# Kernel optimization log

Hardware: AMD Instinct MI355X
Metric: run time of the kernel (lower is better)

Reference implementation:

```python
import jax, jax.numpy as jnp
import numpy as np

B, L, H, NH, HD, DI, NL = 8, 4096, 256, 4, 64, 1024, 6
_SCALE = 1.0 / np.sqrt(HD).astype(np.float32)


def _layernorm(x, g, b, eps=1e-5):
    m = x.mean(-1, keepdims=True)
    v = ((x - m) ** 2).mean(-1, keepdims=True)
    return (x - m) / jnp.sqrt(v + eps) * g + b


def _forward(data, mask, pos_emb, ln_g, ln_b, ff_w1, ff_b1, ff_w2, ff_b2,
             ff_lng, ff_lnb, ring_wq, ring_bq, ring_wk, ring_bk, ring_wv,
             ring_bv, ring_wo, ring_bo, star_wq, star_bq, star_wk, star_bk,
             star_wv, star_bv, star_wo, star_bo):
    pad = ~mask                                         # [B,L] True = padding
    spad = jnp.concatenate([jnp.zeros((B, 1), bool), pad], axis=1)  # [B,L+1]
    x = data + pos_emb[None, :L]                        # [B,L,H] (emb dropout = eval identity)
    nodes = x
    relay = x.mean(axis=1)                              # [B,H]
    for i in range(NL):
        # --- PositionwiseFeedForward (1x1 conv == dense over channels) ---
        h = nodes
        t = jax.nn.relu(h @ ff_w1[i].T + ff_b1[i]) @ ff_w2[i].T + ff_b2[i]
        h = _layernorm(t + h, ff_lng[i], ff_lnb[i])     # [B,L,H]
        # --- ring attention (_MSA1): size-3 sliding window + global relay key ---
        q = (h @ ring_wq[i].T + ring_bq[i]).reshape(B, L, NH, HD)
        k = (h @ ring_wk[i].T + ring_bk[i]).reshape(B, L, NH, HD)
        v = (h @ ring_wv[i].T + ring_bv[i]).reshape(B, L, NH, HD)
        kp = jnp.pad(k, ((0, 0), (1, 1), (0, 0), (0, 0)))  # zero pad, matches F.unfold
        vp = jnp.pad(v, ((0, 0), (1, 1), (0, 0), (0, 0)))
        k_win = jnp.stack([kp[:, 0:L], kp[:, 1:L + 1], kp[:, 2:L + 2]], axis=2)  # [B,L,3,NH,HD]
        v_win = jnp.stack([vp[:, 0:L], vp[:, 1:L + 1], vp[:, 2:L + 2]], axis=2)
        ak = (relay @ ring_wk[i].T + ring_bk[i]).reshape(B, 1, 1, NH, HD)
        av = (relay @ ring_wv[i].T + ring_bv[i]).reshape(B, 1, 1, NH, HD)
        k_all = jnp.concatenate([k_win, jnp.broadcast_to(ak, (B, L, 1, NH, HD))], axis=2)
        v_all = jnp.concatenate([v_win, jnp.broadcast_to(av, (B, L, 1, NH, HD))], axis=2)
        scores = jnp.einsum('blnd,blwnd->blwn', q, k_all) * _SCALE
        alphas = jax.nn.softmax(scores, axis=2)         # softmax over window dim (4)
        att = jnp.einsum('blwn,blwnd->blnd', alphas, v_all).reshape(B, L, NH * HD)
        ring_out = att @ ring_wo[i].T + ring_bo[i]
        nodes = jax.nn.leaky_relu(_layernorm(ring_out, ln_g[i], ln_b[i]))
        # --- star attention (_MSA2): relay attends to [relay; nodes] ---
        y = jnp.concatenate([relay[:, None, :], nodes], axis=1)  # [B,L+1,H]
        sq = (relay @ star_wq[i].T + star_bq[i]).reshape(B, NH, HD)
        sk = (y @ star_wk[i].T + star_bk[i]).reshape(B, L + 1, NH, HD)
        sv = (y @ star_wv[i].T + star_bv[i]).reshape(B, L + 1, NH, HD)
        s = jnp.einsum('bnd,blnd->bnl', sq, sk) * _SCALE
        s = jnp.where(spad[:, None, :], -jnp.inf, s)
        a = jax.nn.softmax(s, axis=-1)
        satt = jnp.einsum('bnl,blnd->bnd', a, sv).reshape(B, NH * HD)
        relay = jax.nn.leaky_relu(satt @ star_wo[i].T + star_bo[i])
        nodes = jnp.where(pad[:, :, None], 0.0, nodes)
    return nodes, relay


def setup_inputs() -> dict:
    key = jax.random.key(0)
    ks = iter(jax.random.split(key, 64))
    p = lambda shape: jax.random.normal(next(ks), shape, jnp.float32) * 0.02
    C = NH * HD
    return dict(
        data=jax.random.normal(next(ks), (B, L, H), jnp.float32),
        mask=jnp.ones((B, L), bool),
        pos_emb=p((L, H)),
        ln_g=jnp.ones((NL, H), jnp.float32), ln_b=jnp.zeros((NL, H), jnp.float32),
        ff_w1=p((NL, DI, H)), ff_b1=jnp.zeros((NL, DI), jnp.float32),
        ff_w2=p((NL, H, DI)), ff_b2=jnp.zeros((NL, H), jnp.float32),
        ff_lng=jnp.ones((NL, H), jnp.float32), ff_lnb=jnp.zeros((NL, H), jnp.float32),
        ring_wq=p((NL, C, H)), ring_bq=jnp.zeros((NL, C), jnp.float32),
        ring_wk=p((NL, C, H)), ring_bk=jnp.zeros((NL, C), jnp.float32),
        ring_wv=p((NL, C, H)), ring_bv=jnp.zeros((NL, C), jnp.float32),
        ring_wo=p((NL, H, C)), ring_bo=jnp.zeros((NL, H), jnp.float32),
        star_wq=p((NL, C, H)), star_bq=jnp.zeros((NL, C), jnp.float32),
        star_wk=p((NL, C, H)), star_bk=jnp.zeros((NL, C), jnp.float32),
        star_wv=p((NL, C, H)), star_bv=jnp.zeros((NL, C), jnp.float32),
        star_wo=p((NL, H, C)), star_bo=jnp.zeros((NL, H), jnp.float32),
    )


def reference(data, mask, pos_emb, ln_g, ln_b, ff_w1, ff_b1, ff_w2, ff_b2,
              ff_lng, ff_lnb, ring_wq, ring_bq, ring_wk, ring_bk, ring_wv,
              ring_bv, ring_wo, ring_bo, star_wq, star_bq, star_wk, star_bk,
              star_wv, star_bv, star_wo, star_bo):
    return _forward(data, mask, pos_emb, ln_g, ln_b, ff_w1, ff_b1, ff_w2,
                    ff_b2, ff_lng, ff_lnb, ring_wq, ring_bq, ring_wk, ring_bk,
                    ring_wv, ring_bv, ring_wo, ring_bo, star_wq, star_bq,
                    star_wk, star_bk, star_wv, star_bv, star_wo, star_bo)
```

## Files before the change

### kernel.cpp

```cpp
#include <hip/hip_runtime.h>
#include <hip/hip_bf16.h>

#define B_ 8
#define L_ 4096
#define H_ 256
#define NH_ 4
#define DI_ 1024
#define NL_ 6
#define TOK_ (B_*L_)

typedef unsigned short u16;
typedef __attribute__((ext_vector_type(8))) short short8;
typedef __attribute__((ext_vector_type(4))) float f32x4;

struct __align__(8) u16x4 { u16 x,y,z,w; };

__device__ __forceinline__ float bf2f(u16 u){
  union { unsigned u; float f; } c; c.u = ((unsigned)u)<<16; return c.f;
}
__device__ __forceinline__ u16 f2bf(float f){
  union { float f; unsigned u; } c; c.f = f;
  unsigned r = c.u + 0x7FFF + ((c.u>>16)&1);
  return (u16)(r>>16);
}
__device__ __forceinline__ void gload_lds16(const short* g, short* l){
  __builtin_amdgcn_global_load_lds(
      (const __attribute__((address_space(1))) void*)g,
      (__attribute__((address_space(3))) void*)l, 16, 0, 0);
}
__device__ __forceinline__ void block_sync(){
  asm volatile("" ::: "memory");
  __builtin_amdgcn_s_barrier();
  __builtin_amdgcn_sched_barrier(0);
}
#define WAIT_VMCNT(N) asm volatile("s_waitcnt vmcnt(" #N ")" ::: "memory")
#define WAIT_LGKM0()  asm volatile("s_waitcnt lgkmcnt(0)" ::: "memory")

template<bool RELU, bool OBF16>
__global__ __launch_bounds__(512, 4) void gemm_bt(
    const u16* __restrict__ A, const u16* __restrict__ W,
    const float* __restrict__ bias, void* __restrict__ out, int N, int K, int nbn)
{
  constexpr int BM=128, BK=64;
  __shared__ __align__(16) short As[2][BM*BK];
  __shared__ __align__(16) short Ws[2][BM*BK];
  const int tid = threadIdx.x, lane = tid&63, wid = tid>>6;
  const int wm = wid>>1, wn = wid&1;
  const int id = blockIdx.x;
  const int xcd = id & 7, j = id >> 3;
  const int bm = xcd*32 + j / nbn;
  const int bn = j % nbn;
  const short* Ag = (const short*)A + (size_t)bm*BM*K;
  const short* Wg = (const short*)W + (size_t)bn*BM*K;
  f32x4 acc[2][4] = {};

  auto STAGE = [&](int k0, int buf){
    #pragma unroll
    for (int jj=0;jj<2;++jj){
      int c = jj*512 + tid;
      int row = c>>3;
      int col = (c&7) ^ (row&7);
      const size_t src = (size_t)row*K + k0 + col*8;
      gload_lds16(Ag + src, &As[buf][(size_t)c*8]);
      gload_lds16(Wg + src, &Ws[buf][(size_t)c*8]);
    }
  };
  auto COMPUTE = [&](int cur){
    #pragma unroll
    for (int kk=0;kk<BK;kk+=32){
      short8 af[2], bfr[4];
      int kc = (kk>>3) + (lane>>4);
      #pragma unroll
      for (int ms=0;ms<2;++ms){
        int r = wm*32 + ms*16 + (lane&15);
        af[ms] = *(const short8*)&As[cur][r*BK + ((kc ^ (r&7))<<3)];
      }
      #pragma unroll
      for (int ns=0;ns<4;++ns){
        int r = wn*64 + ns*16 + (lane&15);
        bfr[ns] = *(const short8*)&Ws[cur][r*BK + ((kc ^ (r&7))<<3)];
      }
      #pragma unroll
      for (int ms=0;ms<2;++ms)
        #pragma unroll
        for (int ns=0;ns<4;++ns)
          acc[ms][ns] = __builtin_amdgcn_mfma_f32_16x16x32_bf16(af[ms], bfr[ns], acc[ms][ns], 0, 0, 0);
    }
  };

  const int NT = K/BK;
  STAGE(0, 0); STAGE(BK, 1);
  WAIT_VMCNT(4);
  block_sync();
  for (int t=0;t<NT;++t){
    const int cur = t&1;
    __builtin_amdgcn_s_setprio(1);
    COMPUTE(cur);
    __builtin_amdgcn_s_setprio(0);
    block_sync();
    if (t+2 < NT) STAGE((t+2)*BK, cur);
    if (t+1 < NT){
      if (t+2 < NT) { WAIT_VMCNT(4); }
      else          { WAIT_VMCNT(0); }
      block_sync();
    }
  }
  if (OBF16){
    constexpr int OP = 136;
    u16* O = (u16*)&As[0][0];
    #pragma unroll
    for (int ns=0;ns<4;++ns){
      int lc = wn*64 + ns*16 + (lane&15);
      float bc = bias[bn*BM + lc];
      #pragma unroll
      for (int ms=0;ms<2;++ms){
        int rbase = wm*32 + ms*16 + ((lane>>4)<<2);
        #pragma unroll
        for (int i=0;i<4;++i){
          float v = acc[ms][ns][i] + bc;
          if (RELU) v = fmaxf(v, 0.f);
          O[(rbase+i)*OP + lc] = f2bf(v);
        }
      }
    }
    block_sync();
    u16* ob = (u16*)out + (size_t)bm*BM*N + bn*BM;
    const int rr = tid>>4;
    const int cc = (tid&15)<<3;
    #pragma unroll
    for (int p=0;p<4;++p){
      int r = p*32 + rr;
      *reinterpret_cast<short8*>(ob + (size_t)r*N + cc) =
          *reinterpret_cast<const short8*>(&O[r*OP + cc]);
    }
  } else {
    const int r0 = bm*BM + wm*32;
    const int c0 = bn*BM + wn*64;
    #pragma unroll
    for (int ns=0;ns<4;++ns){
      int col = c0 + ns*16 + (lane&15);
      float bc = bias[col];
      #pragma unroll
      for (int ms=0;ms<2;++ms){
        int rbase = r0 + ms*16 + ((lane>>4)<<2);
        #pragma unroll
        for (int i=0;i<4;++i){
          float v = acc[ms][ns][i] + bc;
          if (RELU) v = fmaxf(v, 0.f);
          ((float*)out)[(size_t)(rbase+i)*N + col] = v;
        }
      }
    }
  }
}

template<bool ADDRES, bool LEAKY>
__global__ __launch_bounds__(512, 4) void gemm_ln(
    const u16* __restrict__ A, const u16* __restrict__ W,
    const float* __restrict__ bias, const u16* __restrict__ res,
    const float* __restrict__ g, const float* __restrict__ bv,
    u16* __restrict__ outb, float* __restrict__ outf, int K)
{
  constexpr int BM=64, BK=64;
  __shared__ __align__(16) short As[2][BM*BK];
  __shared__ __align__(16) short Ws[2][256*BK];
  float* S1  = (float*)&As[0][0];
  float* S2  = S1 + 64*4;
  float* MU  = S2 + 64*4;
  float* RSD = MU + 64;
  const int tid = threadIdx.x, lane = tid&63, wid = tid>>6;
  const int wm = wid>>2, wn = wid&3;
  const int m0 = blockIdx.x*BM;
  const short* Ag = (const short*)A + (size_t)m0*K;
  const short* Wg = (const short*)W;
  f32x4 acc[2][4] = {};

  auto STAGE = [&](int k0, int buf){
    {
      int c = tid;
      int row = c>>3;
      int col = (c&7) ^ (row&7);
      gload_lds16(Ag + (size_t)row*K + k0 + col*8, &As[buf][(size_t)c*8]);
    }
    #pragma unroll
    for (int jj=0;jj<4;++jj){
      int c = jj*512 + tid;
      int row = c>>3;
      int col = (c&7) ^ (row&7);
      gload_lds16(Wg + (size_t)row*K + k0 + col*8, &Ws[buf][(size_t)c*8]);
    }
  };
  auto COMPUTE = [&](int cur){
    #pragma unroll
    for (int kk=0;kk<BK;kk+=32){
      short8 af[2], bfr[4];
      int kc = (kk>>3) + (lane>>4);
      #pragma unroll
      for (int ms=0;ms<2;++ms){
        int r = wm*32 + ms*16 + (lane&15);
        af[ms] = *(const short8*)&As[cur][r*BK + ((kc ^ (r&7))<<3)];
      }
      #pragma unroll
      for (int ns=0;ns<4;++ns){
        int r = wn*64 + ns*16 + (lane&15);
        bfr[ns] = *(const short8*)&Ws[cur][r*BK + ((kc ^ (r&7))<<3)];
      }
      #pragma unroll
      for (int ms=0;ms<2;++ms)
        #pragma unroll
        for (int ns=0;ns<4;++ns)
          acc[ms][ns] = __builtin_amdgcn_mfma_f32_16x16x32_bf16(af[ms], bfr[ns], acc[ms][ns], 0, 0, 0);
    }
  };

  const int NT = K/BK;
  STAGE(0, 0); STAGE(BK, 1);
  WAIT_VMCNT(5);
  block_sync();
  for (int t=0;t<NT;++t){
    const int cur = t&1;
    __builtin_amdgcn_s_setprio(1);
    COMPUTE(cur);
    __builtin_amdgcn_s_setprio(0);
    block_sync();
    if (t+2 < NT) STAGE((t+2)*BK, cur);
    if (t+1 < NT){
      if (t+2 < NT) { WAIT_VMCNT(5); }
      else          { WAIT_VMCNT(0); }
      block_sync();
    }
  }
  #pragma unroll
  for (int ns=0;ns<4;++ns){
    int col = wn*64 + ns*16 + (lane&15);
    float bc = bias[col];
    #pragma unroll
    for (int ms=0;ms<2;++ms){
      int rl = wm*32 + ms*16 + ((lane>>4)<<2);
      #pragma unroll
      for (int i=0;i<4;++i){
        float v = acc[ms][ns][i] + bc;
        if (ADDRES) v += bf2f(res[(size_t)(m0+rl+i)*256 + col]);
        acc[ms][ns][i] = v;
      }
    }
  }
  #pragma unroll
  for (int ms=0;ms<2;++ms)
    #pragma unroll
    for (int i=0;i<4;++i){
      float p1 = acc[ms][0][i]+acc[ms][1][i]+acc[ms][2][i]+acc[ms][3][i];
      float p2 = acc[ms][0][i]*acc[ms][0][i] + acc[ms][1][i]*acc[ms][1][i]
               + acc[ms][2][i]*acc[ms][2][i] + acc[ms][3][i]*acc[ms][3][i];
      #pragma unroll
      for (int o=1;o<16;o<<=1){ p1 += __shfl_xor(p1,o,64); p2 += __shfl_xor(p2,o,64); }
      if ((lane&15)==0){
        int rl = wm*32 + ms*16 + ((lane>>4)<<2) + i;
        S1[rl*4 + wn] = p1; S2[rl*4 + wn] = p2;
      }
    }
  __syncthreads();
  if (tid < 64){
    float s1 = S1[tid*4+0]+S1[tid*4+1]+S1[tid*4+2]+S1[tid*4+3];
    float s2 = S2[tid*4+0]+S2[tid*4+1]+S2[tid*4+2]+S2[tid*4+3];
    float mean = s1*(1.f/256.f);
    float var = fmaxf(s2*(1.f/256.f) - mean*mean, 0.f);
    MU[tid] = mean; RSD[tid] = 1.f/sqrtf(var + 1e-5f);
  }
  __syncthreads();
  constexpr int OP = 268;
  u16* O = (u16*)&Ws[0][0];
  #pragma unroll
  for (int ns=0;ns<4;++ns){
    int col = wn*64 + ns*16 + (lane&15);
    float gg = g[col], bb = bv[col];
    #pragma unroll
    for (int ms=0;ms<2;++ms){
      int rl = wm*32 + ms*16 + ((lane>>4)<<2);
      #pragma unroll
      for (int i=0;i<4;++i){
        float y = (acc[ms][ns][i] - MU[rl+i])*RSD[rl+i]*gg + bb;
        if (LEAKY) y = y>0.f ? y : 0.01f*y;
        O[(rl+i)*OP + col] = f2bf(y);
        if (outf) outf[(size_t)(m0+rl+i)*256 + col] = y;
      }
    }
  }
  __syncthreads();
  u16* ob = outb + (size_t)m0*256;
  const int rr = tid>>5;
  const int cc = (tid&31)<<3;
  #pragma unroll
  for (int p=0;p<4;++p){
    int r = p*16 + rr;
    *reinterpret_cast<short8*>(ob + ((size_t)r<<8) + cc) =
        *reinterpret_cast<const short8*>(&O[r*OP + cc]);
  }
}

__global__ __launch_bounds__(512, 4) void attn_ln(
    const u16* __restrict__ qkv, const float* __restrict__ akav,
    const u16* __restrict__ W, const float* __restrict__ bo,
    const float* __restrict__ g, const float* __restrict__ bv,
    u16* __restrict__ outb, float* __restrict__ outf)
{
  constexpr int BK=32, NT=256/BK;
  __shared__ __align__(16) char LB[74240];
  short* Afull = (short*)LB;
  short* Ws2   = (short*)(LB + 32768);
  float* S1  = (float*)(LB + 65536);
  float* S2  = S1 + 256;
  float* MU  = S2 + 256;
  float* RSD = MU + 64;
  const int tid = threadIdx.x, lane = tid&63, wid = tid>>6;
  const int wm = wid>>2, wn = wid&3;
  const int m0 = blockIdx.x*64;
  const short* Wg = (const short*)W;

  auto STAGE_W = [&](int k0, int buf){
    #pragma unroll
    for (int jj=0;jj<2;++jj){
      int c = jj*512 + tid;
      int row = c>>2;
      int col = (c&3) ^ (row&3);
      gload_lds16(Wg + (size_t)row*256 + k0 + col*8, &Ws2[(size_t)buf*8192 + (size_t)c*8]);
    }
  };

  STAGE_W(0, 0); STAGE_W(BK, 1);
  __builtin_amdgcn_sched_barrier(0);

  for (int it=0; it<8; ++it){
    const int rl = wid*8 + it;
    const size_t tok = (size_t)(m0 + rl);
    const int l = (int)(tok & (L_-1));
    const int b = (int)(tok >> 12);
    float q[4], kp[4], kc[4], kn[4], ak[4], vp[4], vc[4], vn[4], av[4];
    u16x4 t4 = *(const u16x4*)(qkv + tok*768 + lane*4);
    q[0]=bf2f(t4.x); q[1]=bf2f(t4.y); q[2]=bf2f(t4.z); q[3]=bf2f(t4.w);
    t4 = *(const u16x4*)(qkv + tok*768 + 256 + lane*4);
    kc[0]=bf2f(t4.x); kc[1]=bf2f(t4.y); kc[2]=bf2f(t4.z); kc[3]=bf2f(t4.w);
    t4 = *(const u16x4*)(qkv + tok*768 + 512 + lane*4);
    vc[0]=bf2f(t4.x); vc[1]=bf2f(t4.y); vc[2]=bf2f(t4.z); vc[3]=bf2f(t4.w);
    if (l>0){
      t4 = *(const u16x4*)(qkv + (tok-1)*768 + 256 + lane*4);
      kp[0]=bf2f(t4.x); kp[1]=bf2f(t4.y); kp[2]=bf2f(t4.z); kp[3]=bf2f(t4.w);
      t4 = *(const u16x4*)(qkv + (tok-1)*768 + 512 + lane*4);
      vp[0]=bf2f(t4.x); vp[1]=bf2f(t4.y); vp[2]=bf2f(t4.z); vp[3]=bf2f(t4.w);
    } else { kp[0]=kp[1]=kp[2]=kp[3]=0.f; vp[0]=vp[1]=vp[2]=vp[3]=0.f; }
    if (l<L_-1){
      t4 = *(const u16x4*)(qkv + (tok+1)*768 + 256 + lane*4);
      kn[0]=bf2f(t4.x); kn[1]=bf2f(t4.y); kn[2]=bf2f(t4.z); kn[3]=bf2f(t4.w);
      t4 = *(const u16x4*)(qkv + (tok+1)*768 + 512 + lane*4);
      vn[0]=bf2f(t4.x); vn[1]=bf2f(t4.y); vn[2]=bf2f(t4.z); vn[3]=bf2f(t4.w);
    } else { kn[0]=kn[1]=kn[2]=kn[3]=0.f; vn[0]=vn[1]=vn[2]=vn[3]=0.f; }
    float4 f4 = ((const float4*)(akav + (size_t)b*H_))[lane];
    ak[0]=f4.x; ak[1]=f4.y; ak[2]=f4.z; ak[3]=f4.w;
    f4 = ((const float4*)(akav + 2048 + (size_t)b*H_))[lane];
    av[0]=f4.x; av[1]=f4.y; av[2]=f4.z; av[3]=f4.w;
    float dp=0.f, dc=0.f, dn=0.f, da=0.f;
    #pragma unroll
    for (int jc=0;jc<4;++jc){ dp += q[jc]*kp[jc]; dc += q[jc]*kc[jc]; dn += q[jc]*kn[jc]; da += q[jc]*ak[jc]; }
    #pragma unroll
    for (int o=1;o<16;o<<=1){
      dp += __shfl_xor(dp,o,64); dc += __shfl_xor(dc,o,64);
      dn += __shfl_xor(dn,o,64); da += __shfl_xor(da,o,64);
    }
    dp *= 0.125f; dc *= 0.125f; dn *= 0.125f; da *= 0.125f;
    float m = fmaxf(fmaxf(dp,dc), fmaxf(dn,da));
    float e0 = expf(dp-m), e1 = expf(dc-m), e2 = expf(dn-m), e3 = expf(da-m);
    float rd = 1.f/(e0+e1+e2+e3);
    u16x4 o4;
    o4.x = f2bf((e0*vp[0]+e1*vc[0]+e2*vn[0]+e3*av[0])*rd);
    o4.y = f2bf((e0*vp[1]+e1*vc[1]+e2*vn[1]+e3*av[1])*rd);
    o4.z = f2bf((e0*vp[2]+e1*vc[2]+e2*vn[2]+e3*av[2])*rd);
    o4.w = f2bf((e0*vp[3]+e1*vc[3]+e2*vn[3]+e3*av[3])*rd);
    int gq = lane>>1;
    int s = (gq & ~7) | ((gq&7) ^ (rl&7));
    *(u16x4*)&Afull[rl*256 + s*8 + (lane&1)*4] = o4;
  }
  WAIT_LGKM0();
  WAIT_VMCNT(2);
  block_sync();

  f32x4 acc[2][4] = {};
  for (int t=0;t<NT;++t){
    const int cur = t&1;
    __builtin_amdgcn_s_setprio(1);
    {
      short8 af[2], bfr[4];
      #pragma unroll
      for (int ms=0;ms<2;++ms){
        int r = wm*32 + ms*16 + (lane&15);
        int gk = t*4 + (lane>>4);
        int s = (gk & ~7) | ((gk&7) ^ (r&7));
        af[ms] = *(const short8*)&Afull[r*256 + s*8];
      }
      #pragma unroll
      for (int ns=0;ns<4;++ns){
        int r2 = wn*64 + ns*16 + (lane&15);
        int sl = (lane>>4) ^ (r2&3);
        bfr[ns] = *(const short8*)&Ws2[(size_t)cur*8192 + r2*32 + sl*8];
      }
      #pragma unroll
      for (int ms=0;ms<2;++ms)
        #pragma unroll
        for (int ns=0;ns<4;++ns)
          acc[ms][ns] = __builtin_amdgcn_mfma_f32_16x16x32_bf16(af[ms], bfr[ns], acc[ms][ns], 0, 0, 0);
    }
    __builtin_amdgcn_s_setprio(0);
    block_sync();
    if (t+2 < NT) STAGE_W((t+2)*BK, cur);
    if (t+1 < NT){
      if (t+2 < NT) { WAIT_VMCNT(2); }
      else          { WAIT_VMCNT(0); }
      block_sync();
    }
  }

  #pragma unroll
  for (int ns=0;ns<4;++ns){
    int col = wn*64 + ns*16 + (lane&15);
    float bc = bo[col];
    #pragma unroll
    for (int ms=0;ms<2;++ms)
      #pragma unroll
      for (int i=0;i<4;++i)
        acc[ms][ns][i] += bc;
  }
  #pragma unroll
  for (int ms=0;ms<2;++ms)
    #pragma unroll
    for (int i=0;i<4;++i){
      float p1 = acc[ms][0][i]+acc[ms][1][i]+acc[ms][2][i]+acc[ms][3][i];
      float p2 = acc[ms][0][i]*acc[ms][0][i] + acc[ms][1][i]*acc[ms][1][i]
               + acc[ms][2][i]*acc[ms][2][i] + acc[ms][3][i]*acc[ms][3][i];
      #pragma unroll
      for (int o=1;o<16;o<<=1){ p1 += __shfl_xor(p1,o,64); p2 += __shfl_xor(p2,o,64); }
      if ((lane&15)==0){
        int rl = wm*32 + ms*16 + ((lane>>4)<<2) + i;
        S1[rl*4 + wn] = p1; S2[rl*4 + wn] = p2;
      }
    }
  __syncthreads();
  if (tid < 64){
    float s1 = S1[tid*4+0]+S1[tid*4+1]+S1[tid*4+2]+S1[tid*4+3];
    float s2 = S2[tid*4+0]+S2[tid*4+1]+S2[tid*4+2]+S2[tid*4+3];
    float mean = s1*(1.f/256.f);
    float var = fmaxf(s2*(1.f/256.f) - mean*mean, 0.f);
    MU[tid] = mean; RSD[tid] = 1.f/sqrtf(var + 1e-5f);
  }
  __syncthreads();
  constexpr int OP = 268;
  u16* O = (u16*)LB;
  #pragma unroll
  for (int ns=0;ns<4;++ns){
    int col = wn*64 + ns*16 + (lane&15);
    float gg = g[col], bb = bv[col];
    #pragma unroll
    for (int ms=0;ms<2;++ms){
      int rl = wm*32 + ms*16 + ((lane>>4)<<2);
      #pragma unroll
      for (int i=0;i<4;++i){
        float y = (acc[ms][ns][i] - MU[rl+i])*RSD[rl+i]*gg + bb;
        y = y>0.f ? y : 0.01f*y;
        O[(rl+i)*OP + col] = f2bf(y);
        if (outf) outf[(size_t)(m0+rl+i)*256 + col] = y;
      }
    }
  }
  __syncthreads();
  u16* ob = outb + (size_t)m0*256;
  const int rr = tid>>5, cc = (tid&31)<<3;
  #pragma unroll
  for (int p=0;p<4;++p){
    int r = p*16 + rr;
    *reinterpret_cast<short8*>(ob + ((size_t)r<<8) + cc) =
        *reinterpret_cast<const short8*>(&O[r*OP + cc]);
  }
}

__global__ __launch_bounds__(256) void star_scores(
    const u16* __restrict__ skv, const float* __restrict__ sq,
    const float* __restrict__ sk0, float* __restrict__ s)
{
  const int g = blockIdx.x*4 + (threadIdx.x>>6);
  if (g >= B_*(L_+1)) return;
  const int lane = threadIdx.x & 63;
  const int b = g/(L_+1), j = g%(L_+1);
  float4 qv = ((const float4*)(sq + (size_t)b*H_))[lane];
  float k0,k1,k2,k3;
  if (j==0){
    float4 kv = ((const float4*)(sk0 + (size_t)b*H_))[lane];
    k0=kv.x; k1=kv.y; k2=kv.z; k3=kv.w;
  } else {
    u16x4 t = *(const u16x4*)(skv + ((size_t)b*L_ + (j-1))*512 + lane*4);
    k0=bf2f(t.x); k1=bf2f(t.y); k2=bf2f(t.z); k3=bf2f(t.w);
  }
  float d = qv.x*k0 + qv.y*k1 + qv.z*k2 + qv.w*k3;
  #pragma unroll
  for (int o=1;o<16;o<<=1) d += __shfl_xor(d,o,64);
  if ((lane&15)==0)
    s[(size_t)(b*4 + (lane>>4))*(L_+1) + j] = d*0.125f;
}

__global__ __launch_bounds__(1024) void star_softmax(float* __restrict__ s)
{
  const int bh = blockIdx.x;
  float* row = s + (size_t)bh*(L_+1);
  __shared__ float red[1024];
  const int tid = threadIdx.x;
  float m = -1e30f;
  for (int j=tid; j<L_+1; j+=1024) m = fmaxf(m, row[j]);
  red[tid] = m; __syncthreads();
  for (int st=512; st>0; st>>=1){ if (tid<st) red[tid] = fmaxf(red[tid], red[tid+st]); __syncthreads(); }
  m = red[0]; __syncthreads();
  float sum = 0.f;
  for (int j=tid; j<L_+1; j+=1024){ float e = expf(row[j]-m); row[j] = e; sum += e; }
  red[tid] = sum; __syncthreads();
  for (int st=512; st>0; st>>=1){ if (tid<st) red[tid] += red[tid+st]; __syncthreads(); }
  const float rs = 1.f/red[0];
  for (int j=tid; j<L_+1; j+=1024) row[j] *= rs;
}

__global__ __launch_bounds__(256) void star_satt_part(
    const float* __restrict__ a, const u16* __restrict__ skv, float* __restrict__ part)
{
  const int blk = blockIdx.x;
  const int b = blk >> 6, seg = blk & 63;
  const int tid = threadIdx.x, q4 = tid & 63, sub = tid >> 6;
  const int h = q4 >> 4;
  const float* arow = a + (size_t)(b*4 + h)*(L_+1) + 1;
  float a0=0.f,a1=0.f,a2=0.f,a3=0.f;
  const int j0 = seg*64 + sub*16;
  #pragma unroll 4
  for (int jj=j0; jj<j0+16; ++jj){
    u16x4 v = *(const u16x4*)(skv + ((size_t)b*L_ + jj)*512 + 256 + q4*4);
    float al = arow[jj];
    a0 += al*bf2f(v.x); a1 += al*bf2f(v.y); a2 += al*bf2f(v.z); a3 += al*bf2f(v.w);
  }
  __shared__ float red[4][256];
  red[sub][q4*4+0]=a0; red[sub][q4*4+1]=a1; red[sub][q4*4+2]=a2; red[sub][q4*4+3]=a3;
  __syncthreads();
  if (sub==0){
    #pragma unroll
    for (int c=0;c<4;++c){
      int ch = q4*4+c;
      part[(size_t)blk*256 + ch] = red[0][ch]+red[1][ch]+red[2][ch]+red[3][ch];
    }
  }
}

__global__ __launch_bounds__(256) void pack_wT(
    const float* __restrict__ w0, const float* __restrict__ w1,
    const float* __restrict__ w2, const float* __restrict__ w3,
    const float* __restrict__ w4, const float* __restrict__ w5,
    float* __restrict__ T)
{
  __shared__ float tile[32][33];
  const int blk = blockIdx.x;
  const int t = blk & 63, m = blk >> 6;
  const int l = m / 6, w = m % 6;
  const float* srcs[6] = {w0, w1, w2, w3, w4, w5};
  const float* src = srcs[w] + (size_t)l*65536;
  const int r0 = (t>>3)*32, c0 = (t&7)*32;
  const int rr = threadIdx.x >> 5, cc = threadIdx.x & 31;
  #pragma unroll
  for (int p=0;p<4;++p)
    tile[rr + p*8][cc] = src[(size_t)(r0 + rr + p*8)*256 + c0 + cc];
  __syncthreads();
  float* dst = T + (size_t)m*65536;
  #pragma unroll
  for (int p=0;p<4;++p)
    dst[(size_t)(c0 + rr + p*8)*256 + r0 + cc] = tile[cc][rr + p*8];
}

struct TPB { const float* b; float* out; };
struct TPB5 { TPB p[5]; };
__global__ __launch_bounds__(256) void relay_projs(
    const float* __restrict__ relay, const float* __restrict__ TW, TPB5 tp)
{
  const int b = blockIdx.x, w = blockIdx.y, n = threadIdx.x;
  __shared__ float rs[H_];
  rs[n] = relay[b*H_ + n];
  __syncthreads();
  const float* wt = TW + (size_t)w*65536;
  float s = tp.p[w].b[n];
  #pragma unroll 8
  for (int c=0;c<H_;++c) s += rs[c]*wt[(size_t)c*256 + n];
  tp.p[w].out[b*H_+n] = s;
}

__global__ __launch_bounds__(256) void relay_tail_k(
    const float* __restrict__ part, const float* __restrict__ a,
    const float* __restrict__ sv0, const float* __restrict__ TW,
    const float* __restrict__ bo, float* __restrict__ relay, float* __restrict__ outr)
{
  const int b = blockIdx.x, n = threadIdx.x;
  __shared__ float rs[H_];
  const int h = n >> 6;
  float s = a[(size_t)(b*4+h)*(L_+1)] * sv0[b*H_ + n];
  #pragma unroll 8
  for (int g2=0; g2<64; ++g2) s += part[((size_t)b*64+g2)*256 + n];
  rs[n] = s;
  __syncthreads();
  const float* wt = TW + (size_t)5*65536;
  float v = bo[n];
  #pragma unroll 8
  for (int c=0;c<H_;++c) v += rs[c]*wt[(size_t)c*256 + n];
  v = v>0.f ? v : 0.01f*v;
  relay[b*H_+n] = v;
  if (outr) outr[b*H_+n] = v;
}

__global__ void f32_to_bf16_k(const float* __restrict__ s, u16* __restrict__ d, int n){
  for (int i = blockIdx.x*blockDim.x + threadIdx.x; i < n; i += gridDim.x*blockDim.x)
    d[i] = f2bf(s[i]);
}
__global__ void pack_wqkv(const float* __restrict__ wq, const float* __restrict__ wk,
                          const float* __restrict__ wv, u16* __restrict__ dst){
  const int n = NL_*768*H_;
  for (int i = blockIdx.x*blockDim.x + threadIdx.x; i < n; i += gridDim.x*blockDim.x){
    int l = i/(768*H_); int rem = i%(768*H_); int r = rem/H_; int c = rem%H_;
    float v = (r<256) ? wq[((size_t)l*H_ + r)*H_ + c]
            : (r<512) ? wk[((size_t)l*H_ + (r-256))*H_ + c]
                      : wv[((size_t)l*H_ + (r-512))*H_ + c];
    dst[i] = f2bf(v);
  }
}
__global__ void pack_wskv(const float* __restrict__ wk, const float* __restrict__ wv, u16* __restrict__ dst){
  const int n = NL_*512*H_;
  for (int i = blockIdx.x*blockDim.x + threadIdx.x; i < n; i += gridDim.x*blockDim.x){
    int l = i/(512*H_); int rem = i%(512*H_); int r = rem/H_; int c = rem%H_;
    float v = (r<256) ? wk[((size_t)l*H_ + r)*H_ + c]
                      : wv[((size_t)l*H_ + (r-256))*H_ + c];
    dst[i] = f2bf(v);
  }
}
__global__ void pack_biases(const float* __restrict__ bq, const float* __restrict__ bk,
                            const float* __restrict__ bv, float* __restrict__ dqkv,
                            const float* __restrict__ sbk, const float* __restrict__ sbv,
                            float* __restrict__ dskv){
  int i = blockIdx.x*blockDim.x + threadIdx.x;
  if (i < NL_*768){
    int l = i/768, r = i%768;
    dqkv[i] = (r<256) ? bq[l*H_+r] : (r<512) ? bk[l*H_+r-256] : bv[l*H_+r-512];
  }
  if (i < NL_*512){
    int l = i/512, r = i%512;
    dskv[i] = (r<256) ? sbk[l*H_+r] : sbv[l*H_+r-256];
  }
}
__global__ void init_nodes(const float* __restrict__ data, const float* __restrict__ pos, u16* __restrict__ nodes){
  const int total = TOK_*H_/4;
  int i = blockIdx.x*blockDim.x + threadIdx.x;
  if (i >= total) return;
  float4 d = ((const float4*)data)[i];
  float4 p = ((const float4*)pos)[i % (L_*H_/4)];
  u16x4 o; o.x=f2bf(d.x+p.x); o.y=f2bf(d.y+p.y); o.z=f2bf(d.z+p.z); o.w=f2bf(d.w+p.w);
  ((u16x4*)nodes)[i] = o;
}
__global__ void relay_partial(const float* __restrict__ data, const float* __restrict__ pos, float* __restrict__ part){
  const int b = blockIdx.x>>3, seg = blockIdx.x&7, hh = threadIdx.x;
  float s = 0.f;
  for (int l = seg*512; l < seg*512+512; ++l)
    s += data[((size_t)b*L_ + l)*H_ + hh] + pos[(size_t)l*H_ + hh];
  part[blockIdx.x*H_ + hh] = s;
}
__global__ void relay_combine(const float* __restrict__ part, float* __restrict__ relay){
  const int b = blockIdx.x, hh = threadIdx.x;
  float s = 0.f;
  for (int g=0; g<8; ++g) s += part[(b*8+g)*H_ + hh];
  relay[b*H_+hh] = s * (1.0f/L_);
}

extern "C" void kernel_launch(void* const* d_in, const int* in_sizes, int n_in,
                              void* d_out, int out_size, void* d_ws, size_t ws_size,
                              hipStream_t stream)
{
  const float* data   = (const float*)d_in[0];
  const float* pos    = (const float*)d_in[2];
  const float* ln_g   = (const float*)d_in[3];
  const float* ln_b   = (const float*)d_in[4];
  const float* ff_w1  = (const float*)d_in[5];
  const float* ff_b1  = (const float*)d_in[6];
  const float* ff_w2  = (const float*)d_in[7];
  const float* ff_b2  = (const float*)d_in[8];
  const float* ff_lng = (const float*)d_in[9];
  const float* ff_lnb = (const float*)d_in[10];
  const float* ring_wq= (const float*)d_in[11]; const float* ring_bq= (const float*)d_in[12];
  const float* ring_wk= (const float*)d_in[13]; const float* ring_bk= (const float*)d_in[14];
  const float* ring_wv= (const float*)d_in[15]; const float* ring_bv= (const float*)d_in[16];
  const float* ring_wo= (const float*)d_in[17]; const float* ring_bo= (const float*)d_in[18];
  const float* star_wq= (const float*)d_in[19]; const float* star_bq= (const float*)d_in[20];
  const float* star_wk= (const float*)d_in[21]; const float* star_bk= (const float*)d_in[22];
  const float* star_wv= (const float*)d_in[23]; const float* star_bv= (const float*)d_in[24];
  const float* star_wo= (const float*)d_in[25]; const float* star_bo= (const float*)d_in[26];

  char* ws = (char*)d_ws;
  size_t off = 0;
  auto alc = [&](size_t n){ size_t cur = off; off = (cur + n + 255) & ~(size_t)255; return (void*)(ws + cur); };
  u16*  W1B   = (u16*)alc((size_t)NL_*DI_*H_*2);
  u16*  W2B   = (u16*)alc((size_t)NL_*H_*DI_*2);
  u16*  WQKVB = (u16*)alc((size_t)NL_*768*H_*2);
  u16*  WOB   = (u16*)alc((size_t)NL_*H_*H_*2);
  u16*  WSKVB = (u16*)alc((size_t)NL_*512*H_*2);
  float* BQKVB= (float*)alc((size_t)NL_*768*4);
  float* BSKVB= (float*)alc((size_t)NL_*512*4);
  float* TWB  = (float*)alc((size_t)NL_*6*H_*H_*4);
  u16*  NB    = (u16*)alc((size_t)TOK_*H_*2);
  u16*  HB    = (u16*)alc((size_t)TOK_*H_*2);
  u16*  T1R   = (u16*)alc((size_t)TOK_*DI_*2);
  float* RELAY  = (float*)alc(B_*H_*4);
  float* PART   = (float*)alc(64*H_*4);
  float* AKAV   = (float*)alc(2*B_*H_*4);
  float* SQB    = (float*)alc(B_*H_*4);
  float* SK0B   = (float*)alc(B_*H_*4);
  float* SV0B   = (float*)alc(B_*H_*4);
  float* SBUF   = (float*)alc((size_t)B_*NH_*(L_+1)*4);
  float* SPART  = (float*)alc((size_t)B_*64*256*4);
  u16* QKVB = T1R;
  u16* SKVB = T1R;

  f32_to_bf16_k<<<2048, 256, 0, stream>>>(ff_w1, W1B, NL_*DI_*H_);
  f32_to_bf16_k<<<2048, 256, 0, stream>>>(ff_w2, W2B, NL_*H_*DI_);
  f32_to_bf16_k<<<1024, 256, 0, stream>>>(ring_wo, WOB, NL_*H_*H_);
  pack_wqkv<<<2048, 256, 0, stream>>>(ring_wq, ring_wk, ring_wv, WQKVB);
  pack_wskv<<<2048, 256, 0, stream>>>(star_wk, star_wv, WSKVB);
  pack_biases<<<18, 256, 0, stream>>>(ring_bq, ring_bk, ring_bv, BQKVB, star_bk, star_bv, BSKVB);
  pack_wT<<<NL_*6*64, 256, 0, stream>>>(ring_wk, ring_wv, star_wq, star_wk, star_wv, star_wo, TWB);

  init_nodes<<<(TOK_*H_/4 + 255)/256, 256, 0, stream>>>(data, pos, NB);
  relay_partial<<<64, 256, 0, stream>>>(data, pos, PART);
  relay_combine<<<B_, 256, 0, stream>>>(PART, RELAY);

  for (int l=0; l<NL_; ++l){
    const float* TWl = TWB + (size_t)l*6*H_*H_;
    gemm_bt<true,true><<<(DI_/128)*(TOK_/128), 512, 0, stream>>>(
        NB, W1B + (size_t)l*DI_*H_, ff_b1 + l*DI_, T1R, DI_, H_, DI_/128);
    gemm_ln<true,false><<<TOK_/64, 512, 0, stream>>>(
        T1R, W2B + (size_t)l*H_*DI_, ff_b2 + l*H_, NB,
        ff_lng + l*H_, ff_lnb + l*H_, HB, nullptr, DI_);
    TPB5 tp;
    tp.p[0] = { ring_bk + l*H_, AKAV };
    tp.p[1] = { ring_bv + l*H_, AKAV + 2048 };
    tp.p[2] = { star_bq + l*H_, SQB };
    tp.p[3] = { star_bk + l*H_, SK0B };
    tp.p[4] = { star_bv + l*H_, SV0B };
    relay_projs<<<dim3(B_,5), 256, 0, stream>>>(RELAY, TWl, tp);
    gemm_bt<false,true><<<(768/128)*(TOK_/128), 512, 0, stream>>>(
        HB, WQKVB + (size_t)l*768*H_, BQKVB + l*768, QKVB, 768, H_, 768/128);
    attn_ln<<<TOK_/64, 512, 0, stream>>>(
        QKVB, AKAV, WOB + (size_t)l*H_*H_, ring_bo + l*H_,
        ln_g + l*H_, ln_b + l*H_, NB,
        (l==NL_-1) ? (float*)d_out : nullptr);
    gemm_bt<false,true><<<(512/128)*(TOK_/128), 512, 0, stream>>>(
        NB, WSKVB + (size_t)l*512*H_, BSKVB + l*512, SKVB, 512, H_, 512/128);
    star_scores<<<(B_*(L_+1) + 3)/4, 256, 0, stream>>>(SKVB, SQB, SK0B, SBUF);
    star_softmax<<<B_*NH_, 1024, 0, stream>>>(SBUF);
    star_satt_part<<<B_*64, 256, 0, stream>>>(SBUF, SKVB, SPART);
    relay_tail_k<<<B_, 256, 0, stream>>>(SPART, SBUF, SV0B, TWl,
        star_bo + l*H_, RELAY,
        (l==NL_-1) ? ((float*)d_out + (size_t)TOK_*H_) : nullptr);
  }
}
```

Measured before the change: 1.072 ms.

## Fuse star attention scores into KV GEMM epilogue and defer softmax normalization

The star-key/value GEMM epilogue now computes the query-key dot products per token and head straight from the accumulators and writes the scaled scores, which removes the separate star_scores kernel and its re-read of the bf16 keys. The softmax kernel is reduced to computing only the max and the reciprocal sum per row, and the exponentials are recomputed on the fly in star_satt_part and relay_tail_k. This saves a full write-back pass over the score buffer and one kernel launch. The cost is extra shuffle reductions in the GEMM epilogue and repeated expf work in the consumers.

```diff
diff --git a/kernel.cpp b/kernel.cpp
--- a/kernel.cpp
+++ b/kernel.cpp
@@ -36,10 +36,11 @@
 #define WAIT_VMCNT(N) asm volatile("s_waitcnt vmcnt(" #N ")" ::: "memory")
 #define WAIT_LGKM0()  asm volatile("s_waitcnt lgkmcnt(0)" ::: "memory")
 
-template<bool RELU, bool OBF16>
+template<bool RELU, bool OBF16, bool SCORES>
 __global__ __launch_bounds__(512, 4) void gemm_bt(
     const u16* __restrict__ A, const u16* __restrict__ W,
-    const float* __restrict__ bias, void* __restrict__ out, int N, int K, int nbn)
+    const float* __restrict__ bias, void* __restrict__ out, int N, int K, int nbn,
+    const float* __restrict__ sq, float* __restrict__ sbuf)
 {
   constexpr int BM=128, BK=64;
   __shared__ __align__(16) short As[2][BM*BK];
@@ -104,6 +105,31 @@
       else          { WAIT_VMCNT(0); }
       block_sync();
     }
+  }
+  if (SCORES && bn < 2){
+    const int b = bm >> 5;
+    const int head = bn*2 + wn;
+    float sqv[4], bcv[4];
+    #pragma unroll
+    for (int ns=0;ns<4;++ns){
+      int lc = wn*64 + ns*16 + (lane&15);
+      sqv[ns] = sq[b*H_ + bn*BM + lc];
+      bcv[ns] = bias[bn*BM + lc];
+    }
+    #pragma unroll
+    for (int ms=0;ms<2;++ms)
+      #pragma unroll
+      for (int i=0;i<4;++i){
+        float p = (acc[ms][0][i]+bcv[0])*sqv[0] + (acc[ms][1][i]+bcv[1])*sqv[1]
+                + (acc[ms][2][i]+bcv[2])*sqv[2] + (acc[ms][3][i]+bcv[3])*sqv[3];
+        #pragma unroll
+        for (int o=1;o<16;o<<=1) p += __shfl_xor(p,o,64);
+        if ((lane&15)==0){
+          int row = wm*32 + ms*16 + ((lane>>4)<<2) + i;
+          int l = (bm*BM + row) & (L_-1);
+          sbuf[(size_t)(b*4 + head)*(L_+1) + 1 + l] = p*0.125f;
+        }
+      }
   }
   if (OBF16){
     constexpr int OP = 136;
@@ -480,63 +506,49 @@
   }
 }
 
-__global__ __launch_bounds__(256) void star_scores(
-    const u16* __restrict__ skv, const float* __restrict__ sq,
-    const float* __restrict__ sk0, float* __restrict__ s)
-{
-  const int g = blockIdx.x*4 + (threadIdx.x>>6);
-  if (g >= B_*(L_+1)) return;
-  const int lane = threadIdx.x & 63;
-  const int b = g/(L_+1), j = g%(L_+1);
-  float4 qv = ((const float4*)(sq + (size_t)b*H_))[lane];
-  float k0,k1,k2,k3;
-  if (j==0){
-    float4 kv = ((const float4*)(sk0 + (size_t)b*H_))[lane];
-    k0=kv.x; k1=kv.y; k2=kv.z; k3=kv.w;
-  } else {
-    u16x4 t = *(const u16x4*)(skv + ((size_t)b*L_ + (j-1))*512 + lane*4);
-    k0=bf2f(t.x); k1=bf2f(t.y); k2=bf2f(t.z); k3=bf2f(t.w);
-  }
-  float d = qv.x*k0 + qv.y*k1 + qv.z*k2 + qv.w*k3;
-  #pragma unroll
-  for (int o=1;o<16;o<<=1) d += __shfl_xor(d,o,64);
-  if ((lane&15)==0)
-    s[(size_t)(b*4 + (lane>>4))*(L_+1) + j] = d*0.125f;
-}
-
-__global__ __launch_bounds__(1024) void star_softmax(float* __restrict__ s)
+__global__ __launch_bounds__(256) void star_maxsum(
+    float* __restrict__ s, const float* __restrict__ sq,
+    const float* __restrict__ sk0, float* __restrict__ sms)
 {
   const int bh = blockIdx.x;
+  const int b = bh>>2, h = bh&3;
   float* row = s + (size_t)bh*(L_+1);
-  __shared__ float red[1024];
+  __shared__ float red[256];
   const int tid = threadIdx.x;
-  float m = -1e30f;
-  for (int j=tid; j<L_+1; j+=1024) m = fmaxf(m, row[j]);
+  float p0 = (tid < 64) ? sq[b*H_ + h*64 + tid]*sk0[b*H_ + h*64 + tid] : 0.f;
+  red[tid] = p0; __syncthreads();
+  for (int st=128; st>0; st>>=1){ if (tid<st) red[tid] += red[tid+st]; __syncthreads(); }
+  const float s0 = red[0]*0.125f;
+  if (tid==0) row[0] = s0;
+  __syncthreads();
+  float m = s0;
+  for (int j=1+tid; j<=L_; j+=256) m = fmaxf(m, row[j]);
   red[tid] = m; __syncthreads();
-  for (int st=512; st>0; st>>=1){ if (tid<st) red[tid] = fmaxf(red[tid], red[tid+st]); __syncthreads(); }
+  for (int st=128; st>0; st>>=1){ if (tid<st) red[tid] = fmaxf(red[tid], red[tid+st]); __syncthreads(); }
   m = red[0]; __syncthreads();
-  float sum = 0.f;
-  for (int j=tid; j<L_+1; j+=1024){ float e = expf(row[j]-m); row[j] = e; sum += e; }
+  float sum = (tid==0) ? expf(s0-m) : 0.f;
+  for (int j=1+tid; j<=L_; j+=256) sum += expf(row[j]-m);
   red[tid] = sum; __syncthreads();
-  for (int st=512; st>0; st>>=1){ if (tid<st) red[tid] += red[tid+st]; __syncthreads(); }
-  const float rs = 1.f/red[0];
-  for (int j=tid; j<L_+1; j+=1024) row[j] *= rs;
+  for (int st=128; st>0; st>>=1){ if (tid<st) red[tid] += red[tid+st]; __syncthreads(); }
+  if (tid==0){ sms[bh*2] = m; sms[bh*2+1] = 1.f/red[0]; }
 }
 
 __global__ __launch_bounds__(256) void star_satt_part(
-    const float* __restrict__ a, const u16* __restrict__ skv, float* __restrict__ part)
+    const float* __restrict__ a, const float* __restrict__ sms,
+    const u16* __restrict__ skv, float* __restrict__ part)
 {
   const int blk = blockIdx.x;
   const int b = blk >> 6, seg = blk & 63;
   const int tid = threadIdx.x, q4 = tid & 63, sub = tid >> 6;
   const int h = q4 >> 4;
   const float* arow = a + (size_t)(b*4 + h)*(L_+1) + 1;
+  const float m = sms[(b*4+h)*2], rs = sms[(b*4+h)*2+1];
   float a0=0.f,a1=0.f,a2=0.f,a3=0.f;
   const int j0 = seg*64 + sub*16;
   #pragma unroll 4
   for (int jj=j0; jj<j0+16; ++jj){
     u16x4 v = *(const u16x4*)(skv + ((size_t)b*L_ + jj)*512 + 256 + q4*4);
-    float al = arow[jj];
+    float al = expf(arow[jj]-m)*rs;
     a0 += al*bf2f(v.x); a1 += al*bf2f(v.y); a2 += al*bf2f(v.z); a3 += al*bf2f(v.w);
   }
   __shared__ float red[4][256];
@@ -593,13 +605,16 @@
 
 __global__ __launch_bounds__(256) void relay_tail_k(
     const float* __restrict__ part, const float* __restrict__ a,
-    const float* __restrict__ sv0, const float* __restrict__ TW,
-    const float* __restrict__ bo, float* __restrict__ relay, float* __restrict__ outr)
+    const float* __restrict__ sms, const float* __restrict__ sv0,
+    const float* __restrict__ TW, const float* __restrict__ bo,
+    float* __restrict__ relay, float* __restrict__ outr)
 {
   const int b = blockIdx.x, n = threadIdx.x;
   __shared__ float rs[H_];
   const int h = n >> 6;
-  float s = a[(size_t)(b*4+h)*(L_+1)] * sv0[b*H_ + n];
+  const float m = sms[(b*4+h)*2], rsum = sms[(b*4+h)*2+1];
+  float a0 = expf(a[(size_t)(b*4+h)*(L_+1)] - m)*rsum;
+  float s = a0 * sv0[b*H_ + n];
   #pragma unroll 8
   for (int g2=0; g2<64; ++g2) s += part[((size_t)b*64+g2)*256 + n];
   rs[n] = s;
@@ -718,6 +733,7 @@
   float* SK0B   = (float*)alc(B_*H_*4);
   float* SV0B   = (float*)alc(B_*H_*4);
   float* SBUF   = (float*)alc((size_t)B_*NH_*(L_+1)*4);
+  float* SMS    = (float*)alc((size_t)B_*NH_*2*4);
   float* SPART  = (float*)alc((size_t)B_*64*256*4);
   u16* QKVB = T1R;
   u16* SKVB = T1R;
@@ -736,8 +752,9 @@
 
   for (int l=0; l<NL_; ++l){
     const float* TWl = TWB + (size_t)l*6*H_*H_;
-    gemm_bt<true,true><<<(DI_/128)*(TOK_/128), 512, 0, stream>>>(
-        NB, W1B + (size_t)l*DI_*H_, ff_b1 + l*DI_, T1R, DI_, H_, DI_/128);
+    gemm_bt<true,true,false><<<(DI_/128)*(TOK_/128), 512, 0, stream>>>(
+        NB, W1B + (size_t)l*DI_*H_, ff_b1 + l*DI_, T1R, DI_, H_, DI_/128,
+        nullptr, nullptr);
     gemm_ln<true,false><<<TOK_/64, 512, 0, stream>>>(
         T1R, W2B + (size_t)l*H_*DI_, ff_b2 + l*H_, NB,
         ff_lng + l*H_, ff_lnb + l*H_, HB, nullptr, DI_);
@@ -748,18 +765,19 @@
     tp.p[3] = { star_bk + l*H_, SK0B };
     tp.p[4] = { star_bv + l*H_, SV0B };
     relay_projs<<<dim3(B_,5), 256, 0, stream>>>(RELAY, TWl, tp);
-    gemm_bt<false,true><<<(768/128)*(TOK_/128), 512, 0, stream>>>(
-        HB, WQKVB + (size_t)l*768*H_, BQKVB + l*768, QKVB, 768, H_, 768/128);
+    gemm_bt<false,true,false><<<(768/128)*(TOK_/128), 512, 0, stream>>>(
+        HB, WQKVB + (size_t)l*768*H_, BQKVB + l*768, QKVB, 768, H_, 768/128,
+        nullptr, nullptr);
     attn_ln<<<TOK_/64, 512, 0, stream>>>(
         QKVB, AKAV, WOB + (size_t)l*H_*H_, ring_bo + l*H_,
         ln_g + l*H_, ln_b + l*H_, NB,
         (l==NL_-1) ? (float*)d_out : nullptr);
-    gemm_bt<false,true><<<(512/128)*(TOK_/128), 512, 0, stream>>>(
-        NB, WSKVB + (size_t)l*512*H_, BSKVB + l*512, SKVB, 512, H_, 512/128);
-    star_scores<<<(B_*(L_+1) + 3)/4, 256, 0, stream>>>(SKVB, SQB, SK0B, SBUF);
-    star_softmax<<<B_*NH_, 1024, 0, stream>>>(SBUF);
-    star_satt_part<<<B_*64, 256, 0, stream>>>(SBUF, SKVB, SPART);
-    relay_tail_k<<<B_, 256, 0, stream>>>(SPART, SBUF, SV0B, TWl,
+    gemm_bt<false,true,true><<<(512/128)*(TOK_/128), 512, 0, stream>>>(
+        NB, WSKVB + (size_t)l*512*H_, BSKVB + l*512, SKVB, 512, H_, 512/128,
+        SQB, SBUF);
+    star_maxsum<<<B_*NH_, 256, 0, stream>>>(SBUF, SQB, SK0B, SMS);
+    star_satt_part<<<B_*64, 256, 0, stream>>>(SBUF, SMS, SKVB, SPART);
+    relay_tail_k<<<B_, 256, 0, stream>>>(SPART, SBUF, SMS, SV0B, TWl,
         star_bo + l*H_, RELAY,
         (l==NL_-1) ? ((float*)d_out + (size_t)TOK_*H_) : nullptr);
   }
```

New measurement: 1.078 ms. About the same (+0.6%).
